# Optimization experiments

Hardware: AMD Instinct MI355X
Metric: run time of the kernel (lower is better)

The kernel has to match this reference:

```python
import jax, jax.numpy as jnp
import numpy as np


def setup_inputs() -> dict:
    key = jax.random.key(0)
    kq, kk, kw, kv = jax.random.split(key, 4)
    B, T, Dq, Dk, A = 32, 4096, 512, 512, 512
    q = jax.random.normal(kq, (B, Dq), dtype=jnp.float32)
    k = jax.random.normal(kk, (B, T, Dk), dtype=jnp.float32)
    # Dense kernel over concat([q, k]) last dim -> attention_size (TruncatedNormal 0.02)
    W = jax.random.truncated_normal(kw, -2.0, 2.0, (Dq + Dk, A), dtype=jnp.float32) * 0.02
    b = jnp.zeros((A,), dtype=jnp.float32)
    # VarianceScaling(scale=2.0, 'normal') over fan_in=A
    v = jax.random.normal(kv, (A,), dtype=jnp.float32) * jnp.sqrt(2.0 / A)
    return {"q": q, "k": k, "W": W, "b": b, "v": v}


def reference(q, k, W, b, v):
    # Original: tile q over T, concat with k, Dense(tanh), dot with v.
    # Equivalent (same math) without materializing the [B,T,Dq+Dk] concat:
    # split W into Wq (rows for q part) and Wk (rows for k part).
    Dq = q.shape[-1]
    Wq, Wk = W[:Dq], W[Dq:]
    qp = q @ Wq                                  # [B, A]
    kp = jnp.einsum('btd,da->bta', k, Wk)        # [B, T, A]
    out = jnp.tanh(qp[:, None, :] + kp + b)      # [B, T, A]
    score = jnp.einsum('bta,a->bt', out, v)      # [B, T]
    return score
```

## Files before the change

### kernel.cpp

```cpp
#include <hip/hip_runtime.h>
#include <hip/hip_bf16.h>
#include <stdint.h>

#define DQ 512
#define DK 512
#define NA 512
#define TT 4096
#define NBATCH 32
#define M_TOTAL (NBATCH * TT)

#define BM 64
#define BK 32
#define KITERS (DK / BK)

typedef __attribute__((ext_vector_type(8))) short bf16x8;
typedef __attribute__((ext_vector_type(4))) float f32x4;

__device__ __forceinline__ void gll16(const void* g, void* l) {
  __builtin_amdgcn_global_load_lds(
      (const __attribute__((address_space(1))) uint32_t*)g,
      (__attribute__((address_space(3))) uint32_t*)l, 16, 0, 0);
}

__device__ __forceinline__ uint32_t pack2bf16(float a, float b) {
  uint32_t ua = __float_as_uint(a) + 0x8000u;
  uint32_t ub = __float_as_uint(b) + 0x8000u;
  return __builtin_amdgcn_perm(ub, ua, 0x07060302);
}

__device__ __forceinline__ float fast_tanh(float x) {
  float e = __expf(2.0f * x);
  return 1.0f - 2.0f * __builtin_amdgcn_rcpf(e + 1.0f);
}

__global__ void prep_kernel(const float* __restrict__ W,
                            const float* __restrict__ q,
                            const float* __restrict__ bias,
                            uint16_t* __restrict__ WkTt,
                            float* __restrict__ qpb) {
  const int tid = threadIdx.x;
  if (blockIdx.x < 64) {
    __shared__ uint16_t T[64][65];
    const int d0 = (blockIdx.x & 7) * 64;
    const int a0 = (blockIdx.x >> 3) * 64;
#pragma unroll
    for (int j = 0; j < 16; ++j) {
      int dd = j * 4 + (tid >> 6);
      int aa = tid & 63;
      uint32_t u = __float_as_uint(W[(size_t)(DQ + d0 + dd) * NA + a0 + aa]) + 0x8000u;
      T[dd][aa] = (uint16_t)(u >> 16);
    }
    __syncthreads();
#pragma unroll
    for (int j = 0; j < 8; ++j) {
      int aa = j * 8 + (tid >> 5);
      int n  = a0 + aa;
      int dp = (tid & 31) * 2;
      int d  = d0 + dp;
      uint32_t val = (uint32_t)T[dp][aa] | ((uint32_t)T[dp + 1][aa] << 16);
      *(uint32_t*)(WkTt + (size_t)(d >> 5) * 16384 + n * 32 + (d & 31)) = val;
    }
  } else {
    const int bb = blockIdx.x - 64;
    const int b  = bb >> 1;
    const int a  = (bb & 1) * 256 + tid;
    const float* qr = q + b * DQ;
    float acc = bias[a];
#pragma unroll 8
    for (int d = 0; d < DQ; ++d)
      acc = fmaf(qr[d], W[(size_t)d * NA + a], acc);
    qpb[b * NA + a] = acc;
  }
}

__global__ __launch_bounds__(512, 4)
void score_kernel(const float* __restrict__ Kmat,
                  const uint16_t* __restrict__ WkTt,
                  const float* __restrict__ qpb,
                  const float* __restrict__ v,
                  float* __restrict__ out) {
  __shared__ __align__(16) uint16_t As[2][BM * BK];
  __shared__ __align__(16) uint16_t Bs[2][NA * BK];
  __shared__ float part[8][BM];

  const int tid  = threadIdx.x;
  const int lane = tid & 63;
  const int w    = tid >> 6;
  const int r16  = lane & 15;
  const int quad = lane >> 4;
  const int m_tile = blockIdx.x;
  const int sw = quad ^ ((r16 >> 1) & 3);

  const float* Ag = Kmat + (size_t)m_tile * BM * DK;

  f32x4 acc[4][4];
#pragma unroll
  for (int i = 0; i < 4; ++i)
#pragma unroll
    for (int j = 0; j < 4; ++j) {
      f32x4 z = {0.f, 0.f, 0.f, 0.f};
      acc[i][j] = z;
    }

  const uint16_t* bsrc[4];
#pragma unroll
  for (int j = 0; j < 4; ++j) {
    int s   = j * 512 + w * 64 + lane;
    int n   = s >> 2;
    int ksl = s & 3;
    int ks  = ksl ^ ((n >> 1) & 3);
    bsrc[j] = WkTt + n * 32 + ks * 8;
  }
  const int bdst_off[4] = { (0 * 512 + w * 64) * 16, (1 * 512 + w * 64) * 16,
                            (2 * 512 + w * 64) * 16, (3 * 512 + w * 64) * 16 };

  const int arow = tid >> 3;
  const int akp  = (tid & 7) * 4;
  const float* Asrc = Ag + (size_t)arow * DK + akp;
  const int As_off = arow * 64 + ((akp >> 3) ^ ((arow >> 1) & 3)) * 16 + (akp & 7) * 2;

#pragma unroll
  for (int j = 0; j < 4; ++j) {
    gll16((const void*)bsrc[j], (void*)((char*)Bs[0] + bdst_off[j]));
    bsrc[j] += 16384;
  }
  {
    float4 c0 = *(const float4*)(Asrc);
    uint2 p;
    p.x = pack2bf16(c0.x, c0.y);
    p.y = pack2bf16(c0.z, c0.w);
    *(uint2*)((char*)As[0] + As_off) = p;
  }
  float4 c = *(const float4*)(Asrc + BK);

#pragma unroll 2
  for (int it = 0; it < KITERS; ++it) {
    const int cur = it & 1, nxt = cur ^ 1;

    __syncthreads();

    if (it + 1 < KITERS) {
#pragma unroll
      for (int j = 0; j < 4; ++j) {
        gll16((const void*)bsrc[j], (void*)((char*)Bs[nxt] + bdst_off[j]));
        bsrc[j] += 16384;
      }
      uint2 p;
      p.x = pack2bf16(c.x, c.y);
      p.y = pack2bf16(c.z, c.w);
      *(uint2*)((char*)As[nxt] + As_off) = p;
      if (it + 2 < KITERS) c = *(const float4*)(Asrc + (it + 2) * BK);
    }

    bf16x8 af[4], bfr[4];
#pragma unroll
    for (int ms = 0; ms < 4; ++ms)
      af[ms] = *(const bf16x8*)((char*)As[cur] + (ms * 16 + r16) * 64 + sw * 16);
#pragma unroll
    for (int ns = 0; ns < 4; ++ns)
      bfr[ns] = *(const bf16x8*)((char*)Bs[cur] + (w * 64 + ns * 16 + r16) * 64 + sw * 16);
#pragma unroll
    for (int ms = 0; ms < 4; ++ms)
#pragma unroll
      for (int ns = 0; ns < 4; ++ns)
        acc[ms][ns] = __builtin_amdgcn_mfma_f32_16x16x32_bf16(
            af[ms], bfr[ns], acc[ms][ns], 0, 0, 0);
  }

  const size_t row0 = (size_t)m_tile * BM;
  const int b_idx = m_tile >> 6;

  float vv[4], qv[4];
#pragma unroll
  for (int ns = 0; ns < 4; ++ns) {
    int a = w * 64 + ns * 16 + r16;
    vv[ns] = v[a];
    qv[ns] = qpb[b_idx * NA + a];
  }

#pragma unroll
  for (int ms = 0; ms < 4; ++ms) {
#pragma unroll
    for (int reg = 0; reg < 4; ++reg) {
      float s = 0.f;
#pragma unroll
      for (int ns = 0; ns < 4; ++ns) {
        float x = acc[ms][ns][reg] + qv[ns];
        s = fmaf(fast_tanh(x), vv[ns], s);
      }
      s += __shfl_xor(s, 1);
      s += __shfl_xor(s, 2);
      s += __shfl_xor(s, 4);
      s += __shfl_xor(s, 8);
      if (r16 == 0) part[w][ms * 16 + quad * 4 + reg] = s;
    }
  }
  __syncthreads();
  if (tid < BM) {
    float s = 0.f;
#pragma unroll
    for (int ww = 0; ww < 8; ++ww) s += part[ww][tid];
    out[row0 + tid] = s;
  }
}

extern "C" void kernel_launch(void* const* d_in, const int* in_sizes, int n_in,
                              void* d_out, int out_size, void* d_ws, size_t ws_size,
                              hipStream_t stream) {
  const float* q = (const float*)d_in[0];
  const float* k = (const float*)d_in[1];
  const float* W = (const float*)d_in[2];
  const float* b = (const float*)d_in[3];
  const float* v = (const float*)d_in[4];
  float* out = (float*)d_out;

  float* qpb = (float*)d_ws;
  uint16_t* WkTt = (uint16_t*)((char*)d_ws + 65536);

  prep_kernel<<<128, 256, 0, stream>>>(W, q, b, WkTt, qpb);
  score_kernel<<<M_TOTAL / BM, 512, 0, stream>>>(k, WkTt, qpb, v, out);
}
```

Baseline: 436.7 us.

## Make score kernel persistent with 128-row tiles and triple-buffered B pipeline

Replaces the one-tile-per-block launch (2048 blocks of 512 threads, 64 rows) with 256 persistent blocks of 1024 threads. Each block loops over 128-row tiles and runs one continuous K pipeline across tiles, with the B operand triple-buffered and explicit vmcnt waits in place of full syncthreads. The aim is to remove per-block prologue and epilogue bubbles and to halve how often the Wk tile is reloaded per row. In exchange, occupancy is lower (one large block per CU, more LDS), and the epilogue plus its barrier now stall the pipeline inside the loop.

```diff
diff --git a/kernel.cpp b/kernel.cpp
--- a/kernel.cpp
+++ b/kernel.cpp
@@ -1,17 +1,18 @@
 #include <hip/hip_runtime.h>
-#include <hip/hip_bf16.h>
 #include <stdint.h>
 
 #define DQ 512
 #define DK 512
 #define NA 512
-#define TT 4096
 #define NBATCH 32
-#define M_TOTAL (NBATCH * TT)
-
-#define BM 64
+#define M_TOTAL (NBATCH * 4096)
+
+#define BM 128
 #define BK 32
 #define KITERS (DK / BK)
+#define NBLK 256
+#define ROUNDS (M_TOTAL / (BM * NBLK))
+#define NT (ROUNDS * KITERS)
 
 typedef __attribute__((ext_vector_type(8))) short bf16x8;
 typedef __attribute__((ext_vector_type(4))) float f32x4;
@@ -73,134 +74,144 @@
   }
 }
 
-__global__ __launch_bounds__(512, 4)
+__global__ __launch_bounds__(1024, 4)
 void score_kernel(const float* __restrict__ Kmat,
                   const uint16_t* __restrict__ WkTt,
                   const float* __restrict__ qpb,
                   const float* __restrict__ v,
                   float* __restrict__ out) {
-  __shared__ __align__(16) uint16_t As[2][BM * BK];
-  __shared__ __align__(16) uint16_t Bs[2][NA * BK];
+  __shared__ __align__(16) uint16_t Bs[3 * NA * BK];
+  __shared__ __align__(16) uint16_t As[2 * BM * BK];
   __shared__ float part[8][BM];
 
   const int tid  = threadIdx.x;
   const int lane = tid & 63;
   const int w    = tid >> 6;
+  const int wc   = w & 7;
+  const int wr   = w >> 3;
   const int r16  = lane & 15;
   const int quad = lane >> 4;
-  const int m_tile = blockIdx.x;
-  const int sw = quad ^ ((r16 >> 1) & 3);
-
-  const float* Ag = Kmat + (size_t)m_tile * BM * DK;
-
-  f32x4 acc[4][4];
-#pragma unroll
-  for (int i = 0; i < 4; ++i)
-#pragma unroll
-    for (int j = 0; j < 4; ++j) {
-      f32x4 z = {0.f, 0.f, 0.f, 0.f};
-      acc[i][j] = z;
-    }
-
-  const uint16_t* bsrc[4];
-#pragma unroll
-  for (int j = 0; j < 4; ++j) {
-    int s   = j * 512 + w * 64 + lane;
-    int n   = s >> 2;
-    int ksl = s & 3;
-    int ks  = ksl ^ ((n >> 1) & 3);
-    bsrc[j] = WkTt + n * 32 + ks * 8;
-  }
-  const int bdst_off[4] = { (0 * 512 + w * 64) * 16, (1 * 512 + w * 64) * 16,
-                            (2 * 512 + w * 64) * 16, (3 * 512 + w * 64) * 16 };
+  const int sw   = quad ^ ((r16 >> 1) & 3);
+  const int bid  = blockIdx.x;
+
+  const uint16_t* bconst0;
+  const uint16_t* bconst1;
+  {
+    int s0 = tid;         int n0 = s0 >> 2, k0 = (s0 & 3) ^ ((n0 >> 1) & 3);
+    int s1 = 1024 + tid;  int n1 = s1 >> 2, k1 = (s1 & 3) ^ ((n1 >> 1) & 3);
+    bconst0 = WkTt + n0 * 32 + k0 * 8;
+    bconst1 = WkTt + n1 * 32 + k1 * 8;
+  }
+  const int bdst0 = (0 * 1024 + w * 64) * 16;
+  const int bdst1 = (1 * 1024 + w * 64) * 16;
 
   const int arow = tid >> 3;
   const int akp  = (tid & 7) * 4;
-  const float* Asrc = Ag + (size_t)arow * DK + akp;
-  const int As_off = arow * 64 + ((akp >> 3) ^ ((arow >> 1) & 3)) * 16 + (akp & 7) * 2;
-
-#pragma unroll
-  for (int j = 0; j < 4; ++j) {
-    gll16((const void*)bsrc[j], (void*)((char*)Bs[0] + bdst_off[j]));
-    bsrc[j] += 16384;
-  }
+  const int As_off = arow * 64 + (((akp >> 3) ^ ((arow >> 1) & 3)) * 16) + (akp & 7) * 2;
+  const float* ap = Kmat + (size_t)bid * BM * DK + (size_t)arow * DK + akp;
+
+  const int a_ro = (wr * 64 + r16) * 64 + sw * 16;
+  const int b_ro = (wc * 64 + r16) * 64 + sw * 16;
+
+  f32x4 acc[4][4];
+#pragma unroll
+  for (int i = 0; i < 4; ++i)
+#pragma unroll
+    for (int j = 0; j < 4; ++j) { f32x4 z = {0.f, 0.f, 0.f, 0.f}; acc[i][j] = z; }
+
+  float vv[4];
+#pragma unroll
+  for (int ns = 0; ns < 4; ++ns) vv[ns] = v[wc * 64 + ns * 16 + r16];
+
+  float4 c = *(const float4*)ap;
+  ap += BK;
+  gll16((const void*)bconst0, (void*)((char*)Bs + bdst0));
+  gll16((const void*)bconst1, (void*)((char*)Bs + bdst1));
+  asm volatile("s_waitcnt vmcnt(2)" ::: "memory");
   {
-    float4 c0 = *(const float4*)(Asrc);
-    uint2 p;
-    p.x = pack2bf16(c0.x, c0.y);
-    p.y = pack2bf16(c0.z, c0.w);
-    *(uint2*)((char*)As[0] + As_off) = p;
-  }
-  float4 c = *(const float4*)(Asrc + BK);
-
-#pragma unroll 2
-  for (int it = 0; it < KITERS; ++it) {
-    const int cur = it & 1, nxt = cur ^ 1;
-
-    __syncthreads();
-
-    if (it + 1 < KITERS) {
-#pragma unroll
-      for (int j = 0; j < 4; ++j) {
-        gll16((const void*)bsrc[j], (void*)((char*)Bs[nxt] + bdst_off[j]));
-        bsrc[j] += 16384;
-      }
-      uint2 p;
-      p.x = pack2bf16(c.x, c.y);
-      p.y = pack2bf16(c.z, c.w);
-      *(uint2*)((char*)As[nxt] + As_off) = p;
-      if (it + 2 < KITERS) c = *(const float4*)(Asrc + (it + 2) * BK);
-    }
-
+    uint2 p; p.x = pack2bf16(c.x, c.y); p.y = pack2bf16(c.z, c.w);
+    *(uint2*)((char*)As + As_off) = p;
+  }
+  c = *(const float4*)ap;
+  ap += BK;
+  gll16((const void*)(bconst0 + 16384), (void*)((char*)Bs + 32768 + bdst0));
+  gll16((const void*)(bconst1 + 16384), (void*)((char*)Bs + 32768 + bdst1));
+
+  int rdB = 0;
+#pragma unroll 1
+  for (int t = 0; t < NT; ++t) {
+    if (t < NT - 1)
+      asm volatile("s_waitcnt vmcnt(2) lgkmcnt(0)" ::: "memory");
+    else
+      asm volatile("s_waitcnt vmcnt(0) lgkmcnt(0)" ::: "memory");
+    __builtin_amdgcn_s_barrier();
+
+    if (t + 1 < NT) {
+      uint2 p; p.x = pack2bf16(c.x, c.y); p.y = pack2bf16(c.z, c.w);
+      *(uint2*)((char*)As + ((t + 1) & 1) * 8192 + As_off) = p;
+    }
+    if (t + 2 < NT) {
+      c = *(const float4*)ap;
+      ap += BK;
+      if (((t + 3) & 15) == 0) ap += (size_t)NBLK * BM * DK - DK;
+      asm volatile("" ::: "memory");
+      int wrB = rdB + 2; if (wrB >= 3) wrB -= 3;
+      const int itn = (t + 2) & 15;
+      gll16((const void*)(bconst0 + itn * 16384), (void*)((char*)Bs + wrB * 32768 + bdst0));
+      gll16((const void*)(bconst1 + itn * 16384), (void*)((char*)Bs + wrB * 32768 + bdst1));
+    }
+
+    const char* Abase = (const char*)As + (t & 1) * 8192;
+    const char* Bbase = (const char*)Bs + rdB * 32768;
     bf16x8 af[4], bfr[4];
 #pragma unroll
-    for (int ms = 0; ms < 4; ++ms)
-      af[ms] = *(const bf16x8*)((char*)As[cur] + (ms * 16 + r16) * 64 + sw * 16);
-#pragma unroll
-    for (int ns = 0; ns < 4; ++ns)
-      bfr[ns] = *(const bf16x8*)((char*)Bs[cur] + (w * 64 + ns * 16 + r16) * 64 + sw * 16);
+    for (int ms = 0; ms < 4; ++ms) af[ms] = *(const bf16x8*)(Abase + a_ro + ms * 1024);
+#pragma unroll
+    for (int ns = 0; ns < 4; ++ns) bfr[ns] = *(const bf16x8*)(Bbase + b_ro + ns * 1024);
 #pragma unroll
     for (int ms = 0; ms < 4; ++ms)
 #pragma unroll
       for (int ns = 0; ns < 4; ++ns)
         acc[ms][ns] = __builtin_amdgcn_mfma_f32_16x16x32_bf16(
             af[ms], bfr[ns], acc[ms][ns], 0, 0, 0);
-  }
-
-  const size_t row0 = (size_t)m_tile * BM;
-  const int b_idx = m_tile >> 6;
-
-  float vv[4], qv[4];
-#pragma unroll
-  for (int ns = 0; ns < 4; ++ns) {
-    int a = w * 64 + ns * 16 + r16;
-    vv[ns] = v[a];
-    qv[ns] = qpb[b_idx * NA + a];
-  }
-
-#pragma unroll
-  for (int ms = 0; ms < 4; ++ms) {
-#pragma unroll
-    for (int reg = 0; reg < 4; ++reg) {
-      float s = 0.f;
-#pragma unroll
-      for (int ns = 0; ns < 4; ++ns) {
-        float x = acc[ms][ns][reg] + qv[ns];
-        s = fmaf(fast_tanh(x), vv[ns], s);
+
+    if ((t & 15) == 15) {
+      const int tile  = bid + (t >> 4) * NBLK;
+      const int b_idx = tile >> 5;
+      float qv[4];
+#pragma unroll
+      for (int ns = 0; ns < 4; ++ns) qv[ns] = qpb[b_idx * NA + wc * 64 + ns * 16 + r16];
+#pragma unroll
+      for (int ms = 0; ms < 4; ++ms) {
+#pragma unroll
+        for (int reg = 0; reg < 4; ++reg) {
+          float s = 0.f;
+#pragma unroll
+          for (int ns = 0; ns < 4; ++ns) {
+            float x = acc[ms][ns][reg] + qv[ns];
+            s = fmaf(fast_tanh(x), vv[ns], s);
+          }
+          s += __shfl_xor(s, 1);
+          s += __shfl_xor(s, 2);
+          s += __shfl_xor(s, 4);
+          s += __shfl_xor(s, 8);
+          if (r16 == 0) part[wc][wr * 64 + ms * 16 + quad * 4 + reg] = s;
+        }
       }
-      s += __shfl_xor(s, 1);
-      s += __shfl_xor(s, 2);
-      s += __shfl_xor(s, 4);
-      s += __shfl_xor(s, 8);
-      if (r16 == 0) part[w][ms * 16 + quad * 4 + reg] = s;
-    }
-  }
-  __syncthreads();
-  if (tid < BM) {
-    float s = 0.f;
-#pragma unroll
-    for (int ww = 0; ww < 8; ++ww) s += part[ww][tid];
-    out[row0 + tid] = s;
+      asm volatile("s_waitcnt lgkmcnt(0)" ::: "memory");
+      __builtin_amdgcn_s_barrier();
+      if (tid < BM) {
+        float s = 0.f;
+#pragma unroll
+        for (int cg = 0; cg < 8; ++cg) s += part[cg][tid];
+        out[(size_t)tile * BM + tid] = s;
+      }
+#pragma unroll
+      for (int i = 0; i < 4; ++i)
+#pragma unroll
+        for (int j = 0; j < 4; ++j) { f32x4 z = {0.f, 0.f, 0.f, 0.f}; acc[i][j] = z; }
+    }
+    rdB += 1; if (rdB == 3) rdB = 0;
   }
 }
 
@@ -218,5 +229,5 @@
   uint16_t* WkTt = (uint16_t*)((char*)d_ws + 65536);
 
   prep_kernel<<<128, 256, 0, stream>>>(W, q, b, WkTt, qpb);
-  score_kernel<<<M_TOTAL / BM, 512, 0, stream>>>(k, WkTt, qpb, v, out);
-}
+  score_kernel<<<NBLK, 1024, 0, stream>>>(k, WkTt, qpb, v, out);
+}
```

Result: no change. 434.4 us (-0.5%).
